# Performance work log

Measured on AMD Instinct MI355X. Metric: run time of the kernel, lower is better.

Reference implementation:

```python
import jax, jax.numpy as jnp
import numpy as np

SEQ = 4096
EMB = 2048
DQ = 2048
DV = 2048

def setup_inputs() -> dict:
    key = jax.random.key(0)
    k1, k2, k3, k4 = jax.random.split(key, 4)
    scale = 1.0 / np.sqrt(EMB)
    return {
        "embedding_word": jax.random.normal(k1, (SEQ, EMB), dtype=jnp.float32),
        "w_q": jax.random.normal(k2, (DQ, EMB), dtype=jnp.float32) * scale,
        "w_k": jax.random.normal(k3, (DQ, EMB), dtype=jnp.float32) * scale,
        "w_v": jax.random.normal(k4, (DV, EMB), dtype=jnp.float32) * scale,
    }

def reference(embedding_word, w_q, w_k, w_v):
    # nn.Linear: y = x @ W.T (bias=False)
    q = embedding_word @ w_q.T            # [S, d_q]
    k = embedding_word @ w_k.T            # [S, d_q]
    v = embedding_word @ w_v.T            # [S, d_v]
    scores = q @ k.T                      # [S, S]
    S = scores.shape[0]
    causal = jnp.tril(jnp.ones((S, S), dtype=bool))  # True = keep
    masked = jnp.where(causal, scores, -jnp.inf)
    weights = jax.nn.softmax(masked / jnp.sqrt(jnp.float32(DQ)), axis=-1)
    return weights @ v                    # [S, d_v]
```

## Files before the change

### kernel.cpp

```cpp
#include <hip/hip_runtime.h>


using u16 = unsigned short;
typedef __bf16 bf16x8 __attribute__((ext_vector_type(8)));
typedef float  f32x4  __attribute__((ext_vector_type(4)));
typedef u16    u16x8  __attribute__((ext_vector_type(8)));

__device__ __forceinline__ u16 f2b(float f) {
  union { float f; unsigned u; } x; x.f = f;
  unsigned r = x.u + 0x7fffu + ((x.u >> 16) & 1u);
  return (u16)(r >> 16);
}
__device__ __forceinline__ float b2f(u16 h) {
  union { unsigned u; float f; } x; x.u = ((unsigned)h) << 16;
  return x.f;
}

#define GLL16(src, dst)                                                        \
  __builtin_amdgcn_global_load_lds(                                            \
      (const __attribute__((address_space(1))) void*)(src),                    \
      (__attribute__((address_space(3))) void*)(dst), 16, 0, 0)

#define MFMA_BF16(a, b, c) __builtin_amdgcn_mfma_f32_16x16x32_bf16(a, b, c, 0, 0, 0)

__global__ __launch_bounds__(256)
void cast_all(const float* __restrict__ x, const float* __restrict__ wq,
              const float* __restrict__ wk, const float* __restrict__ wv,
              u16* __restrict__ dst) {
  const int b = blockIdx.x;
  const float* src;
  size_t off;
  if (b < 4096)      { src = x;  off = (size_t)b * 2048; }
  else if (b < 6144) { src = wq; off = (size_t)(b - 4096) * 2048; }
  else if (b < 8192) { src = wk; off = (size_t)(b - 6144) * 2048; }
  else               { src = wv; off = (size_t)(b - 8192) * 2048; }
  const size_t e = off + (size_t)threadIdx.x * 8;
  float4 a = *(const float4*)(src + e);
  float4 c = *(const float4*)(src + e + 4);
  u16x8 o;
  o[0] = f2b(a.x); o[1] = f2b(a.y); o[2] = f2b(a.z); o[3] = f2b(a.w);
  o[4] = f2b(c.x); o[5] = f2b(c.y); o[6] = f2b(c.z); o[7] = f2b(c.w);
  *(u16x8*)(dst + (size_t)b * 2048 + (size_t)threadIdx.x * 8) = o;
}

__global__ __launch_bounds__(512)
void gemm_qk256(const u16* __restrict__ A, const u16* __restrict__ W,
                u16* __restrict__ Qo, u16* __restrict__ Ko) {
  extern __shared__ char lds[];
  constexpr int NT = 32;
  const int bn = blockIdx.x, bm = blockIdx.y;
  const int tid = threadIdx.x;
  const int w = tid >> 6, lane = tid & 63;
  const int wr = w >> 2, wc = w & 3;
  const int l15 = lane & 15, l4 = lane >> 4;
  const int rs = lane >> 3;
  const int csw = ((lane & 7) ^ rs) << 3;
  const int m0 = bm * 256, n0 = bn * 256;

  const u16* gA = A + (size_t)(m0 + w * 8 + rs) * 2048 + csw;
  const u16* gB = W + (size_t)(n0 + w * 8 + rs) * 2048 + csw;
  char* lw = lds + w * 1024;
  const u16* sm = (const u16*)lds;

  auto stA = [&](int p, int u, int tt) {
    GLL16(gA + (size_t)(u * 64) * 2048 + tt * 64, lw + p * 65536 + u * 8192);
  };
  auto stB = [&](int p, int u, int tt) {
    GLL16(gB + (size_t)(u * 64) * 2048 + tt * 64,
          lw + p * 65536 + 32768 + u * 8192);
  };
  const int swz = (l15 & 7) << 3;
  auto rdA = [&](int p, int m, int kk) -> bf16x8 {
    int u = wr * 2 + (m >> 2);
    int r64 = (m & 3) * 16 + l15;
    int e = p * 32768 + u * 4096 + ((r64 * 64 + kk * 32 + l4 * 8) ^ swz);
    return *(const bf16x8*)&sm[e];
  };
  auto rdB = [&](int p, int n, int kk) -> bf16x8 {
    int e = p * 32768 + 16384 + wc * 4096 +
            (((n * 16 + l15) * 64 + kk * 32 + l4 * 8) ^ swz);
    return *(const bf16x8*)&sm[e];
  };

  f32x4 acc[8][4] = {};
  bf16x8 a0[4][2], a1[4][2], b0[2][2], b1[2][2];

  stA(0,0,0); stA(0,1,0); stA(0,2,0); stA(0,3,0);
  stB(0,0,0); stB(0,1,0); stB(0,2,0); stB(0,3,0);
  stA(1,0,1); stA(1,1,1); stA(1,2,1); stA(1,3,1);
  stB(1,0,1); stB(1,1,1); stB(1,2,1); stB(1,3,1);
  asm volatile("s_waitcnt vmcnt(8)" ::: "memory");
  __builtin_amdgcn_sched_barrier(0);
  __builtin_amdgcn_s_barrier();
#pragma unroll
  for (int m = 0; m < 4; ++m) { a0[m][0] = rdA(0,m,0); a0[m][1] = rdA(0,m,1); }
#pragma unroll
  for (int n = 0; n < 2; ++n) { b0[n][0] = rdB(0,n,0); b0[n][1] = rdB(0,n,1); }

  for (int t = 0; t < NT; ++t) {
    const int p = t & 1;
    const bool pre = (t + 2 < NT);
    b1[0][0] = rdB(p,2,0); b1[0][1] = rdB(p,2,1);
    b1[1][0] = rdB(p,3,0); b1[1][1] = rdB(p,3,1);
    a1[0][0] = rdA(p,4,0); a1[0][1] = rdA(p,4,1);
    asm volatile("s_waitcnt lgkmcnt(6)" ::: "memory");
    __builtin_amdgcn_sched_barrier(0);
    __builtin_amdgcn_s_setprio(1);
#pragma unroll
    for (int m = 0; m < 4; ++m)
#pragma unroll
      for (int n = 0; n < 2; ++n)
#pragma unroll
        for (int kk = 0; kk < 2; ++kk)
          acc[m][n] = MFMA_BF16(a0[m][kk], b0[n][kk], acc[m][n]);
    __builtin_amdgcn_s_setprio(0);
    __builtin_amdgcn_s_barrier();
    if (pre) { stA(p, 0, t + 2); stA(p, 2, t + 2); }
    a1[1][0] = rdA(p,5,0); a1[1][1] = rdA(p,5,1);
    a1[2][0] = rdA(p,6,0); a1[2][1] = rdA(p,6,1);
    a1[3][0] = rdA(p,7,0); a1[3][1] = rdA(p,7,1);
    asm volatile("s_waitcnt lgkmcnt(6)" ::: "memory");
    __builtin_amdgcn_sched_barrier(0);
    __builtin_amdgcn_s_setprio(1);
#pragma unroll
    for (int m = 0; m < 4; ++m)
#pragma unroll
      for (int n = 0; n < 2; ++n)
#pragma unroll
        for (int kk = 0; kk < 2; ++kk)
          acc[m][n + 2] = MFMA_BF16(a0[m][kk], b1[n][kk], acc[m][n + 2]);
    __builtin_amdgcn_s_setprio(0);
    __builtin_amdgcn_s_barrier();
    if (pre) { stB(p, 0, t + 2); stB(p, 1, t + 2); stB(p, 2, t + 2); stB(p, 3, t + 2); }
    asm volatile("s_waitcnt lgkmcnt(0)" ::: "memory");
    __builtin_amdgcn_sched_barrier(0);
    __builtin_amdgcn_s_setprio(1);
#pragma unroll
    for (int m = 0; m < 4; ++m)
#pragma unroll
      for (int n = 0; n < 2; ++n)
#pragma unroll
        for (int kk = 0; kk < 2; ++kk)
          acc[m + 4][n] = MFMA_BF16(a1[m][kk], b0[n][kk], acc[m + 4][n]);
    __builtin_amdgcn_s_setprio(0);
    __builtin_amdgcn_s_barrier();
    if (pre) { stA(p, 1, t + 2); stA(p, 3, t + 2); }
    __builtin_amdgcn_s_setprio(1);
#pragma unroll
    for (int m = 0; m < 4; ++m)
#pragma unroll
      for (int n = 0; n < 2; ++n)
#pragma unroll
        for (int kk = 0; kk < 2; ++kk)
          acc[m + 4][n + 2] = MFMA_BF16(a1[m][kk], b1[n][kk], acc[m + 4][n + 2]);
    __builtin_amdgcn_s_setprio(0);
    if (pre)             { asm volatile("s_waitcnt vmcnt(8)" ::: "memory"); }
    else if (t + 1 < NT) { asm volatile("s_waitcnt vmcnt(0)" ::: "memory"); }
    __builtin_amdgcn_sched_barrier(0);
    __builtin_amdgcn_s_barrier();
    if (t + 1 < NT) {
      const int pn = p ^ 1;
#pragma unroll
      for (int m = 0; m < 4; ++m) { a0[m][0] = rdA(pn,m,0); a0[m][1] = rdA(pn,m,1); }
#pragma unroll
      for (int n = 0; n < 2; ++n) { b0[n][0] = rdB(pn,n,0); b0[n][1] = rdB(pn,n,1); }
    }
  }

  const int row0 = m0 + wr * 128 + l4 * 4;
  if (bn < 8) {
    const int cg0 = bn * 256 + wc * 64 + l15;
#pragma unroll
    for (int m = 0; m < 8; ++m)
#pragma unroll
      for (int n = 0; n < 4; ++n)
#pragma unroll
        for (int j = 0; j < 4; ++j)
          Qo[(size_t)(row0 + m * 16 + j) * 2048 + cg0 + n * 16] = f2b(acc[m][n][j]);
  } else {
    const int cg0 = bn * 256 - 2048 + wc * 64 + l15;
#pragma unroll
    for (int m = 0; m < 8; ++m)
#pragma unroll
      for (int n = 0; n < 4; ++n)
#pragma unroll
        for (int j = 0; j < 4; ++j)
          Ko[(size_t)(row0 + m * 16 + j) * 2048 + cg0 + n * 16] = f2b(acc[m][n][j]);
  }
}

__global__ __launch_bounds__(512)
void gemm_qkv(const u16* __restrict__ A, const u16* __restrict__ W,
              u16* __restrict__ Qo, u16* __restrict__ Ko,
              u16* __restrict__ VTo, int bn_base) {
  extern __shared__ char lds[];
  constexpr int NT = 32;
  const int bn = blockIdx.x + bn_base, bm = blockIdx.y;
  const int tid = threadIdx.x;
  const int w = tid >> 6, lane = tid & 63;
  const int wr = w >> 1, wc = w & 1;
  const int l15 = lane & 15, l4 = lane >> 4;
  const int rs = lane >> 3;
  const int csw = ((lane & 7) ^ rs) << 3;
  const int m0 = bm * 256, n0 = bn * 128;

  const u16* gA = A + (size_t)(m0 + w * 8 + rs) * 2048 + csw;
  const u16* gB = W + (size_t)(n0 + w * 8 + rs) * 2048 + csw;
  char* lw = lds + w * 1024;
  const u16* sm = (const u16*)lds;

  auto stA = [&](int p, int u, int tt) {
    GLL16(gA + (size_t)u * 64 * 2048 + tt * 64, lw + p * 49152 + u * 8192);
  };
  auto stB = [&](int p, int u, int tt) {
    GLL16(gB + (size_t)u * 64 * 2048 + tt * 64, lw + p * 49152 + 32768 + u * 8192);
  };
  const int swz = (l15 & 7) << 3;
  auto rdA = [&](int p, int m, int kk) -> bf16x8 {
    int e = p * 24576 + wr * 4096 + (((m * 16 + l15) * 64 + kk * 32 + l4 * 8) ^ swz);
    return *(const bf16x8*)&sm[e];
  };
  auto rdB = [&](int p, int n, int kk) -> bf16x8 {
    int e = p * 24576 + 16384 + wc * 4096 +
            (((n * 16 + l15) * 64 + kk * 32 + l4 * 8) ^ swz);
    return *(const bf16x8*)&sm[e];
  };

  f32x4 acc[4][4] = {};
  bf16x8 aE[4][2], aO[4][2], b01E[2][2], b01O[2][2], b23E[2][2], b23O[2][2];

  stA(0,0,0); stA(0,1,0); stA(0,2,0); stA(0,3,0); stB(0,0,0); stB(0,1,0);
  stA(1,0,1); stA(1,1,1); stA(1,2,1); stA(1,3,1); stB(1,0,1); stB(1,1,1);
  asm volatile("s_waitcnt vmcnt(6)" ::: "memory");
  __builtin_amdgcn_sched_barrier(0);
  __builtin_amdgcn_s_barrier();
#pragma unroll
  for (int m = 0; m < 4; ++m) { aE[m][0] = rdA(0,m,0); aE[m][1] = rdA(0,m,1); }
#pragma unroll
  for (int n = 0; n < 2; ++n) { b01E[n][0] = rdB(0,n,0); b01E[n][1] = rdB(0,n,1); }
  asm volatile("s_waitcnt lgkmcnt(0)" ::: "memory");
  __builtin_amdgcn_sched_barrier(0);
  __builtin_amdgcn_s_barrier();

  for (int i = 0; i < NT / 2; ++i) {
    const int te = 2 * i, to = 2 * i + 1;
    if (te + 2 < NT) { stA(0,0,te+2); stA(0,1,te+2); stA(0,2,te+2); }
#pragma unroll
    for (int n = 0; n < 2; ++n) { b23E[n][0] = rdB(0,n+2,0); b23E[n][1] = rdB(0,n+2,1); }
    __builtin_amdgcn_s_barrier();
    __builtin_amdgcn_s_setprio(1);
#pragma unroll
    for (int m = 0; m < 4; ++m)
#pragma unroll
      for (int n = 0; n < 2; ++n)
#pragma unroll
        for (int kk = 0; kk < 2; ++kk)
          acc[m][n] = MFMA_BF16(aE[m][kk], b01E[n][kk], acc[m][n]);
    __builtin_amdgcn_s_setprio(0);
    asm volatile("s_waitcnt lgkmcnt(0)" ::: "memory");
    __builtin_amdgcn_sched_barrier(0);
    __builtin_amdgcn_s_barrier();
    if (te + 2 < NT) {
      stA(0,3,te+2); stB(0,0,te+2); stB(0,1,te+2);
      asm volatile("s_waitcnt vmcnt(6)" ::: "memory");
    } else {
      asm volatile("s_waitcnt vmcnt(0)" ::: "memory");
    }
    __builtin_amdgcn_sched_barrier(0);
    __builtin_amdgcn_s_barrier();
#pragma unroll
    for (int m = 0; m < 4; ++m) { aO[m][0] = rdA(1,m,0); aO[m][1] = rdA(1,m,1); }
#pragma unroll
    for (int n = 0; n < 2; ++n) { b01O[n][0] = rdB(1,n,0); b01O[n][1] = rdB(1,n,1); }
    __builtin_amdgcn_s_setprio(1);
#pragma unroll
    for (int m = 0; m < 4; ++m)
#pragma unroll
      for (int n = 0; n < 2; ++n)
#pragma unroll
        for (int kk = 0; kk < 2; ++kk)
          acc[m][n+2] = MFMA_BF16(aE[m][kk], b23E[n][kk], acc[m][n+2]);
    __builtin_amdgcn_s_setprio(0);
    asm volatile("s_waitcnt lgkmcnt(0)" ::: "memory");
    __builtin_amdgcn_sched_barrier(0);
    __builtin_amdgcn_s_barrier();
    if (to + 2 < NT) { stA(1,0,to+2); stA(1,1,to+2); stA(1,2,to+2); }
#pragma unroll
    for (int n = 0; n < 2; ++n) { b23O[n][0] = rdB(1,n+2,0); b23O[n][1] = rdB(1,n+2,1); }
    __builtin_amdgcn_s_barrier();
    __builtin_amdgcn_s_setprio(1);
#pragma unroll
    for (int m = 0; m < 4; ++m)
#pragma unroll
      for (int n = 0; n < 2; ++n)
#pragma unroll
        for (int kk = 0; kk < 2; ++kk)
          acc[m][n] = MFMA_BF16(aO[m][kk], b01O[n][kk], acc[m][n]);
    __builtin_amdgcn_s_setprio(0);
    asm volatile("s_waitcnt lgkmcnt(0)" ::: "memory");
    __builtin_amdgcn_sched_barrier(0);
    __builtin_amdgcn_s_barrier();
    if (to + 2 < NT) {
      stA(1,3,to+2); stB(1,0,to+2); stB(1,1,to+2);
      asm volatile("s_waitcnt vmcnt(6)" ::: "memory");
    } else if (to + 1 < NT) {
      asm volatile("s_waitcnt vmcnt(0)" ::: "memory");
    }
    __builtin_amdgcn_sched_barrier(0);
    __builtin_amdgcn_s_barrier();
    if (to + 1 < NT) {
#pragma unroll
      for (int m = 0; m < 4; ++m) { aE[m][0] = rdA(0,m,0); aE[m][1] = rdA(0,m,1); }
#pragma unroll
      for (int n = 0; n < 2; ++n) { b01E[n][0] = rdB(0,n,0); b01E[n][1] = rdB(0,n,1); }
    }
    __builtin_amdgcn_s_setprio(1);
#pragma unroll
    for (int m = 0; m < 4; ++m)
#pragma unroll
      for (int n = 0; n < 2; ++n)
#pragma unroll
        for (int kk = 0; kk < 2; ++kk)
          acc[m][n+2] = MFMA_BF16(aO[m][kk], b23O[n][kk], acc[m][n+2]);
    __builtin_amdgcn_s_setprio(0);
    asm volatile("s_waitcnt lgkmcnt(0)" ::: "memory");
    __builtin_amdgcn_sched_barrier(0);
    __builtin_amdgcn_s_barrier();
  }

  const int row0 = m0 + wr * 64 + l4 * 4;
  const int cg0 = n0 + wc * 64 + l15;
  if (bn < 16) {
#pragma unroll
    for (int m = 0; m < 4; ++m)
#pragma unroll
      for (int n = 0; n < 4; ++n)
#pragma unroll
        for (int j = 0; j < 4; ++j)
          Qo[(size_t)(row0 + m * 16 + j) * 2048 + cg0 + n * 16] = f2b(acc[m][n][j]);
  } else if (bn < 32) {
#pragma unroll
    for (int m = 0; m < 4; ++m)
#pragma unroll
      for (int n = 0; n < 4; ++n)
#pragma unroll
        for (int j = 0; j < 4; ++j)
          Ko[(size_t)(row0 + m * 16 + j) * 2048 + (cg0 + n * 16 - 2048)] = f2b(acc[m][n][j]);
  } else {
#pragma unroll
    for (int m = 0; m < 4; ++m)
#pragma unroll
      for (int n = 0; n < 4; ++n)
#pragma unroll
        for (int j = 0; j < 4; ++j)
          VTo[(size_t)(cg0 + n * 16 - 4096) * 4096 + row0 + m * 16 + j] = f2b(acc[m][n][j]);
  }
}

template<int MODE>
__global__ __launch_bounds__(256)
void pipe128(const u16* __restrict__ A, const u16* __restrict__ B,
             void* __restrict__ C, float alpha) {
  extern __shared__ char lds[];
  constexpr int LDA = (MODE == 0) ? 2048 : 4096;
  constexpr int LDB = (MODE == 0) ? 2048 : 4096;

  int bm, bn, kt0 = 0;
  bool accum = false;
  if (MODE == 0) {
    const int b = blockIdx.x;
    int r = (int)((sqrtf(8.f * (float)b + 1.f) - 1.f) * 0.5f);
    while ((r + 1) * (r + 2) / 2 <= b) ++r;
    while (r * (r + 1) / 2 > b) --r;
    bm = r; bn = b - r * (r + 1) / 2;
  } else if (MODE == 1) {
    bm = 16 + (blockIdx.x >> 4); bn = blockIdx.x & 15;
  } else {
    const int g = blockIdx.x >> 4;
    bn = blockIdx.x & 15;
    if ((g & 1) == 0) { bm = 31 - (g >> 1); kt0 = 32; accum = true; }
    else              { bm = 15 - (g >> 1); }
  }
  const int NT = (MODE == 0 || MODE == 1) ? 32 : (2 * (bm + 1) - kt0);

  const int tid = threadIdx.x;
  const int w = tid >> 6, lane = tid & 63;
  const int wr = w >> 1, wc = w & 1;
  const int l15 = lane & 15, l4 = lane >> 4;
  const int rs = lane >> 3;
  const int csw = ((lane & 7) ^ rs) << 3;
  const int m0 = bm * 128, n0 = bn * 128;

  const u16* gA = A + (size_t)(m0 + w * 8 + rs) * LDA + csw + (size_t)kt0 * 64;
  const u16* gB = B + (size_t)(n0 + w * 8 + rs) * LDB + csw + (size_t)kt0 * 64;
  const u16* gA0 = gA;
  const u16* gA1 = gA + (size_t)32 * LDA;
  const u16* gA2 = gA + (size_t)64 * LDA;
  const u16* gA3 = gA + (size_t)96 * LDA;
  const u16* gB0 = gB;
  const u16* gB1 = gB + (size_t)32 * LDB;
  const u16* gB2 = gB + (size_t)64 * LDB;
  const u16* gB3 = gB + (size_t)96 * LDB;
  char* lw = lds + w * 1024;
  const u16* sm = (const u16*)lds;
#define PDSTA(P, U) (lw + (P) * 32768 + (U) * 4096)
#define PDSTB(P, U) (lw + (P) * 32768 + 16384 + (U) * 4096)

  const int swz = (l15 & 7) << 3;
  auto rdA = [&](int p, int m, int kk) -> bf16x8 {
    int e = p * 16384 + wr * 4096 + (((m * 16 + l15) * 64 + kk * 32 + l4 * 8) ^ swz);
    return *(const bf16x8*)&sm[e];
  };
  auto rdB = [&](int p, int n, int kk) -> bf16x8 {
    int e = p * 16384 + 8192 + wc * 4096 +
            (((n * 16 + l15) * 64 + kk * 32 + l4 * 8) ^ swz);
    return *(const bf16x8*)&sm[e];
  };

  f32x4 acc[4][4] = {};
  bf16x8 aE[4][2], aO[4][2], b01E[2][2], b01O[2][2], b23E[2][2], b23O[2][2];

  GLL16(gA0, PDSTA(0,0)); GLL16(gA1, PDSTA(0,1));
  GLL16(gA2, PDSTA(0,2)); GLL16(gA3, PDSTA(0,3));
  GLL16(gB0, PDSTB(0,0)); GLL16(gB1, PDSTB(0,1));
  GLL16(gB2, PDSTB(0,2)); GLL16(gB3, PDSTB(0,3));
  GLL16(gA0 + 64, PDSTA(1,0)); GLL16(gA1 + 64, PDSTA(1,1));
  GLL16(gA2 + 64, PDSTA(1,2)); GLL16(gA3 + 64, PDSTA(1,3));
  GLL16(gB0 + 64, PDSTB(1,0)); GLL16(gB1 + 64, PDSTB(1,1));
  GLL16(gB2 + 64, PDSTB(1,2)); GLL16(gB3 + 64, PDSTB(1,3));
  gA0 += 128; gA1 += 128; gA2 += 128; gA3 += 128;
  gB0 += 128; gB1 += 128; gB2 += 128; gB3 += 128;
  asm volatile("s_waitcnt vmcnt(8)" ::: "memory");
  __builtin_amdgcn_sched_barrier(0);
  __builtin_amdgcn_s_barrier();
#pragma unroll
  for (int m = 0; m < 4; ++m) { aE[m][0] = rdA(0,m,0); aE[m][1] = rdA(0,m,1); }
#pragma unroll
  for (int n = 0; n < 2; ++n) { b01E[n][0] = rdB(0,n,0); b01E[n][1] = rdB(0,n,1); }
  asm volatile("s_waitcnt lgkmcnt(0)" ::: "memory");
  __builtin_amdgcn_sched_barrier(0);
  __builtin_amdgcn_s_barrier();

  for (int i = 0; i < (NT >> 1); ++i) {
    const int te = 2 * i, to = 2 * i + 1;
    if (te + 2 < NT) { GLL16(gA0, PDSTA(0,0)); GLL16(gA1, PDSTA(0,1));
                       GLL16(gA2, PDSTA(0,2)); GLL16(gA3, PDSTA(0,3)); }
#pragma unroll
    for (int n = 0; n < 2; ++n) { b23E[n][0] = rdB(0,n+2,0); b23E[n][1] = rdB(0,n+2,1); }
    __builtin_amdgcn_s_barrier();
    __builtin_amdgcn_s_setprio(1);
#pragma unroll
    for (int m = 0; m < 4; ++m)
#pragma unroll
      for (int n = 0; n < 2; ++n)
#pragma unroll
        for (int kk = 0; kk < 2; ++kk)
          acc[m][n] = MFMA_BF16(aE[m][kk], b01E[n][kk], acc[m][n]);
    __builtin_amdgcn_s_setprio(0);
    asm volatile("s_waitcnt lgkmcnt(0)" ::: "memory");
    __builtin_amdgcn_sched_barrier(0);
    __builtin_amdgcn_s_barrier();
    if (te + 2 < NT) {
      GLL16(gB0, PDSTB(0,0)); GLL16(gB1, PDSTB(0,1));
      GLL16(gB2, PDSTB(0,2)); GLL16(gB3, PDSTB(0,3));
      asm volatile("s_waitcnt vmcnt(8)" ::: "memory");
    } else {
      asm volatile("s_waitcnt vmcnt(0)" ::: "memory");
    }
    __builtin_amdgcn_sched_barrier(0);
    __builtin_amdgcn_s_barrier();
#pragma unroll
    for (int m = 0; m < 4; ++m) { aO[m][0] = rdA(1,m,0); aO[m][1] = rdA(1,m,1); }
#pragma unroll
    for (int n = 0; n < 2; ++n) { b01O[n][0] = rdB(1,n,0); b01O[n][1] = rdB(1,n,1); }
    __builtin_amdgcn_s_setprio(1);
#pragma unroll
    for (int m = 0; m < 4; ++m)
#pragma unroll
      for (int n = 0; n < 2; ++n)
#pragma unroll
        for (int kk = 0; kk < 2; ++kk)
          acc[m][n+2] = MFMA_BF16(aE[m][kk], b23E[n][kk], acc[m][n+2]);
    __builtin_amdgcn_s_setprio(0);
    asm volatile("s_waitcnt lgkmcnt(0)" ::: "memory");
    __builtin_amdgcn_sched_barrier(0);
    __builtin_amdgcn_s_barrier();
    if (to + 2 < NT) { GLL16(gA0 + 64, PDSTA(1,0)); GLL16(gA1 + 64, PDSTA(1,1));
                       GLL16(gA2 + 64, PDSTA(1,2)); GLL16(gA3 + 64, PDSTA(1,3)); }
#pragma unroll
    for (int n = 0; n < 2; ++n) { b23O[n][0] = rdB(1,n+2,0); b23O[n][1] = rdB(1,n+2,1); }
    __builtin_amdgcn_s_barrier();
    __builtin_amdgcn_s_setprio(1);
#pragma unroll
    for (int m = 0; m < 4; ++m)
#pragma unroll
      for (int n = 0; n < 2; ++n)
#pragma unroll
        for (int kk = 0; kk < 2; ++kk)
          acc[m][n] = MFMA_BF16(aO[m][kk], b01O[n][kk], acc[m][n]);
    __builtin_amdgcn_s_setprio(0);
    asm volatile("s_waitcnt lgkmcnt(0)" ::: "memory");
    __builtin_amdgcn_sched_barrier(0);
    __builtin_amdgcn_s_barrier();
    if (to + 2 < NT) {
      GLL16(gB0 + 64, PDSTB(1,0)); GLL16(gB1 + 64, PDSTB(1,1));
      GLL16(gB2 + 64, PDSTB(1,2)); GLL16(gB3 + 64, PDSTB(1,3));
      asm volatile("s_waitcnt vmcnt(8)" ::: "memory");
    } else if (to + 1 < NT) {
      asm volatile("s_waitcnt vmcnt(0)" ::: "memory");
    }
    __builtin_amdgcn_sched_barrier(0);
    __builtin_amdgcn_s_barrier();
    if (to + 1 < NT) {
#pragma unroll
      for (int m = 0; m < 4; ++m) { aE[m][0] = rdA(0,m,0); aE[m][1] = rdA(0,m,1); }
#pragma unroll
      for (int n = 0; n < 2; ++n) { b01E[n][0] = rdB(0,n,0); b01E[n][1] = rdB(0,n,1); }
    }
    __builtin_amdgcn_s_setprio(1);
#pragma unroll
    for (int m = 0; m < 4; ++m)
#pragma unroll
      for (int n = 0; n < 2; ++n)
#pragma unroll
        for (int kk = 0; kk < 2; ++kk)
          acc[m][n+2] = MFMA_BF16(aO[m][kk], b23O[n][kk], acc[m][n+2]);
    __builtin_amdgcn_s_setprio(0);
    asm volatile("s_waitcnt lgkmcnt(0)" ::: "memory");
    __builtin_amdgcn_sched_barrier(0);
    __builtin_amdgcn_s_barrier();
    gA0 += 128; gA1 += 128; gA2 += 128; gA3 += 128;
    gB0 += 128; gB1 += 128; gB2 += 128; gB3 += 128;
  }
#undef PDSTA
#undef PDSTB

  const int row0 = m0 + wr * 64 + l4 * 4;
  const int col0 = n0 + wc * 64 + l15;
  if (MODE == 0) {
    u16* Co = (u16*)C;
#pragma unroll
    for (int m = 0; m < 4; ++m)
#pragma unroll
      for (int n = 0; n < 4; ++n)
#pragma unroll
        for (int j = 0; j < 4; ++j)
          Co[(size_t)(row0 + m * 16 + j) * 4096 + col0 + n * 16] =
              f2b(acc[m][n][j] * alpha);
  } else {
    float* Co = (float*)C;
    if (MODE == 2 && accum) {
#pragma unroll
      for (int m = 0; m < 4; ++m)
#pragma unroll
        for (int n = 0; n < 4; ++n)
#pragma unroll
          for (int j = 0; j < 4; ++j)
            Co[(size_t)(row0 + m * 16 + j) * 2048 + col0 + n * 16] += acc[m][n][j];
    } else {
#pragma unroll
      for (int m = 0; m < 4; ++m)
#pragma unroll
        for (int n = 0; n < 4; ++n)
#pragma unroll
          for (int j = 0; j < 4; ++j)
            Co[(size_t)(row0 + m * 16 + j) * 2048 + col0 + n * 16] = acc[m][n][j];
    }
  }
}

__global__ __launch_bounds__(256)
void softmax_causal(u16* __restrict__ S) {
  const int i = blockIdx.x;
  const int t = threadIdx.x;
  u16* row = S + (size_t)i * 4096;
  const int L = ((i >> 7) + 1) << 7;
  const bool act = (t * 16) < L;

  u16x8 r0 = {}, r1 = {};
  if (act) {
    r0 = *(const u16x8*)(row + t * 16);
    r1 = *(const u16x8*)(row + t * 16 + 8);
  }

  float v[16];
  float mx = -__builtin_inff();
#pragma unroll
  for (int c = 0; c < 16; ++c) {
    int j = t * 16 + c;
    float x = b2f(c < 8 ? r0[c] : r1[c - 8]);
    v[c] = (j <= i) ? x : -__builtin_inff();
    mx = fmaxf(mx, v[c]);
  }
#pragma unroll
  for (int off = 32; off >= 1; off >>= 1) mx = fmaxf(mx, __shfl_xor(mx, off));
  __shared__ float red[8];
  if ((t & 63) == 0) red[t >> 6] = mx;
  __syncthreads();
  mx = fmaxf(fmaxf(red[0], red[1]), fmaxf(red[2], red[3]));

  float s = 0.f;
#pragma unroll
  for (int c = 0; c < 16; ++c) {
    float e = exp2f((v[c] - mx) * 1.4426950408889634f);
    v[c] = e;
    s += e;
  }
#pragma unroll
  for (int off = 32; off >= 1; off >>= 1) s += __shfl_xor(s, off);
  if ((t & 63) == 0) red[4 + (t >> 6)] = s;
  __syncthreads();
  s = red[4] + red[5] + red[6] + red[7];
  float inv = 1.0f / s;

  if (act) {
    u16x8 o0, o1;
#pragma unroll
    for (int c = 0; c < 8; ++c) {
      o0[c] = f2b(v[c] * inv);
      o1[c] = f2b(v[c + 8] * inv);
    }
    *(u16x8*)(row + t * 16) = o0;
    *(u16x8*)(row + t * 16 + 8) = o1;
  }
}

extern "C" void kernel_launch(void* const* d_in, const int* in_sizes, int n_in,
                              void* d_out, int out_size, void* d_ws, size_t ws_size,
                              hipStream_t stream) {
  const float* x  = (const float*)d_in[0];
  const float* wq = (const float*)d_in[1];
  const float* wk = (const float*)d_in[2];
  const float* wv = (const float*)d_in[3];

  u16* x_bf  = (u16*)d_ws;
  u16* wq_bf = x_bf  + (size_t)4096 * 2048;
  u16* K_bf  = wq_bf + (size_t)3 * 2048 * 2048;
  u16* VT_bf = K_bf  + (size_t)4096 * 2048;
  u16* S_bf  = VT_bf + (size_t)2048 * 4096;
  u16* Q_bf  = (u16*)d_out;

  const float alpha = 0.022097086912079612f;

  cast_all<<<dim3(10240), 256, 0, stream>>>(x, wq, wk, wv, x_bf);

  gemm_qk256<<<dim3(16, 16), 512, 131072, stream>>>(x_bf, wq_bf, Q_bf, K_bf);
  pipe128<0><<<dim3(528), 256, 65536, stream>>>(Q_bf, K_bf, S_bf, alpha);
  gemm_qkv<<<dim3(16, 16), 512, 98304, stream>>>(x_bf, wq_bf, Q_bf, K_bf, VT_bf, 32);
  softmax_causal<<<dim3(4096), 256, 0, stream>>>(S_bf);
  pipe128<1><<<dim3(256), 256, 65536, stream>>>(S_bf, VT_bf, d_out, 1.0f);
  pipe128<2><<<dim3(512), 256, 65536, stream>>>(S_bf, VT_bf, d_out, 1.0f);
}
```

Measured before the change: 237.2 us.

## Merge V^T projection into the QK^T score launch as extra blocks

Removes the separate gemm_qkv launch that produced V^T and instead appends 512 extra blocks to the pipe128<0> QK^T launch. Those blocks compute V^T = Wv · x^T with the 128x128 tile kernel, writing bf16 with a scale of 1. This lets the V projection fill the GPU alongside the causal score tiles instead of running as its own serialized kernel. The trade-off is that V now uses the smaller-tile 256-thread kernel instead of the 256x128 512-thread one, which may lower its per-block efficiency.

```diff
diff --git a/kernel.cpp b/kernel.cpp
--- a/kernel.cpp
+++ b/kernel.cpp
@@ -189,190 +189,34 @@
   }
 }
 
-__global__ __launch_bounds__(512)
-void gemm_qkv(const u16* __restrict__ A, const u16* __restrict__ W,
-              u16* __restrict__ Qo, u16* __restrict__ Ko,
-              u16* __restrict__ VTo, int bn_base) {
-  extern __shared__ char lds[];
-  constexpr int NT = 32;
-  const int bn = blockIdx.x + bn_base, bm = blockIdx.y;
-  const int tid = threadIdx.x;
-  const int w = tid >> 6, lane = tid & 63;
-  const int wr = w >> 1, wc = w & 1;
-  const int l15 = lane & 15, l4 = lane >> 4;
-  const int rs = lane >> 3;
-  const int csw = ((lane & 7) ^ rs) << 3;
-  const int m0 = bm * 256, n0 = bn * 128;
-
-  const u16* gA = A + (size_t)(m0 + w * 8 + rs) * 2048 + csw;
-  const u16* gB = W + (size_t)(n0 + w * 8 + rs) * 2048 + csw;
-  char* lw = lds + w * 1024;
-  const u16* sm = (const u16*)lds;
-
-  auto stA = [&](int p, int u, int tt) {
-    GLL16(gA + (size_t)u * 64 * 2048 + tt * 64, lw + p * 49152 + u * 8192);
-  };
-  auto stB = [&](int p, int u, int tt) {
-    GLL16(gB + (size_t)u * 64 * 2048 + tt * 64, lw + p * 49152 + 32768 + u * 8192);
-  };
-  const int swz = (l15 & 7) << 3;
-  auto rdA = [&](int p, int m, int kk) -> bf16x8 {
-    int e = p * 24576 + wr * 4096 + (((m * 16 + l15) * 64 + kk * 32 + l4 * 8) ^ swz);
-    return *(const bf16x8*)&sm[e];
-  };
-  auto rdB = [&](int p, int n, int kk) -> bf16x8 {
-    int e = p * 24576 + 16384 + wc * 4096 +
-            (((n * 16 + l15) * 64 + kk * 32 + l4 * 8) ^ swz);
-    return *(const bf16x8*)&sm[e];
-  };
-
-  f32x4 acc[4][4] = {};
-  bf16x8 aE[4][2], aO[4][2], b01E[2][2], b01O[2][2], b23E[2][2], b23O[2][2];
-
-  stA(0,0,0); stA(0,1,0); stA(0,2,0); stA(0,3,0); stB(0,0,0); stB(0,1,0);
-  stA(1,0,1); stA(1,1,1); stA(1,2,1); stA(1,3,1); stB(1,0,1); stB(1,1,1);
-  asm volatile("s_waitcnt vmcnt(6)" ::: "memory");
-  __builtin_amdgcn_sched_barrier(0);
-  __builtin_amdgcn_s_barrier();
-#pragma unroll
-  for (int m = 0; m < 4; ++m) { aE[m][0] = rdA(0,m,0); aE[m][1] = rdA(0,m,1); }
-#pragma unroll
-  for (int n = 0; n < 2; ++n) { b01E[n][0] = rdB(0,n,0); b01E[n][1] = rdB(0,n,1); }
-  asm volatile("s_waitcnt lgkmcnt(0)" ::: "memory");
-  __builtin_amdgcn_sched_barrier(0);
-  __builtin_amdgcn_s_barrier();
-
-  for (int i = 0; i < NT / 2; ++i) {
-    const int te = 2 * i, to = 2 * i + 1;
-    if (te + 2 < NT) { stA(0,0,te+2); stA(0,1,te+2); stA(0,2,te+2); }
-#pragma unroll
-    for (int n = 0; n < 2; ++n) { b23E[n][0] = rdB(0,n+2,0); b23E[n][1] = rdB(0,n+2,1); }
-    __builtin_amdgcn_s_barrier();
-    __builtin_amdgcn_s_setprio(1);
-#pragma unroll
-    for (int m = 0; m < 4; ++m)
-#pragma unroll
-      for (int n = 0; n < 2; ++n)
-#pragma unroll
-        for (int kk = 0; kk < 2; ++kk)
-          acc[m][n] = MFMA_BF16(aE[m][kk], b01E[n][kk], acc[m][n]);
-    __builtin_amdgcn_s_setprio(0);
-    asm volatile("s_waitcnt lgkmcnt(0)" ::: "memory");
-    __builtin_amdgcn_sched_barrier(0);
-    __builtin_amdgcn_s_barrier();
-    if (te + 2 < NT) {
-      stA(0,3,te+2); stB(0,0,te+2); stB(0,1,te+2);
-      asm volatile("s_waitcnt vmcnt(6)" ::: "memory");
-    } else {
-      asm volatile("s_waitcnt vmcnt(0)" ::: "memory");
-    }
-    __builtin_amdgcn_sched_barrier(0);
-    __builtin_amdgcn_s_barrier();
-#pragma unroll
-    for (int m = 0; m < 4; ++m) { aO[m][0] = rdA(1,m,0); aO[m][1] = rdA(1,m,1); }
-#pragma unroll
-    for (int n = 0; n < 2; ++n) { b01O[n][0] = rdB(1,n,0); b01O[n][1] = rdB(1,n,1); }
-    __builtin_amdgcn_s_setprio(1);
-#pragma unroll
-    for (int m = 0; m < 4; ++m)
-#pragma unroll
-      for (int n = 0; n < 2; ++n)
-#pragma unroll
-        for (int kk = 0; kk < 2; ++kk)
-          acc[m][n+2] = MFMA_BF16(aE[m][kk], b23E[n][kk], acc[m][n+2]);
-    __builtin_amdgcn_s_setprio(0);
-    asm volatile("s_waitcnt lgkmcnt(0)" ::: "memory");
-    __builtin_amdgcn_sched_barrier(0);
-    __builtin_amdgcn_s_barrier();
-    if (to + 2 < NT) { stA(1,0,to+2); stA(1,1,to+2); stA(1,2,to+2); }
-#pragma unroll
-    for (int n = 0; n < 2; ++n) { b23O[n][0] = rdB(1,n+2,0); b23O[n][1] = rdB(1,n+2,1); }
-    __builtin_amdgcn_s_barrier();
-    __builtin_amdgcn_s_setprio(1);
-#pragma unroll
-    for (int m = 0; m < 4; ++m)
-#pragma unroll
-      for (int n = 0; n < 2; ++n)
-#pragma unroll
-        for (int kk = 0; kk < 2; ++kk)
-          acc[m][n] = MFMA_BF16(aO[m][kk], b01O[n][kk], acc[m][n]);
-    __builtin_amdgcn_s_setprio(0);
-    asm volatile("s_waitcnt lgkmcnt(0)" ::: "memory");
-    __builtin_amdgcn_sched_barrier(0);
-    __builtin_amdgcn_s_barrier();
-    if (to + 2 < NT) {
-      stA(1,3,to+2); stB(1,0,to+2); stB(1,1,to+2);
-      asm volatile("s_waitcnt vmcnt(6)" ::: "memory");
-    } else if (to + 1 < NT) {
-      asm volatile("s_waitcnt vmcnt(0)" ::: "memory");
-    }
-    __builtin_amdgcn_sched_barrier(0);
-    __builtin_amdgcn_s_barrier();
-    if (to + 1 < NT) {
-#pragma unroll
-      for (int m = 0; m < 4; ++m) { aE[m][0] = rdA(0,m,0); aE[m][1] = rdA(0,m,1); }
-#pragma unroll
-      for (int n = 0; n < 2; ++n) { b01E[n][0] = rdB(0,n,0); b01E[n][1] = rdB(0,n,1); }
-    }
-    __builtin_amdgcn_s_setprio(1);
-#pragma unroll
-    for (int m = 0; m < 4; ++m)
-#pragma unroll
-      for (int n = 0; n < 2; ++n)
-#pragma unroll
-        for (int kk = 0; kk < 2; ++kk)
-          acc[m][n+2] = MFMA_BF16(aO[m][kk], b23O[n][kk], acc[m][n+2]);
-    __builtin_amdgcn_s_setprio(0);
-    asm volatile("s_waitcnt lgkmcnt(0)" ::: "memory");
-    __builtin_amdgcn_sched_barrier(0);
-    __builtin_amdgcn_s_barrier();
-  }
-
-  const int row0 = m0 + wr * 64 + l4 * 4;
-  const int cg0 = n0 + wc * 64 + l15;
-  if (bn < 16) {
-#pragma unroll
-    for (int m = 0; m < 4; ++m)
-#pragma unroll
-      for (int n = 0; n < 4; ++n)
-#pragma unroll
-        for (int j = 0; j < 4; ++j)
-          Qo[(size_t)(row0 + m * 16 + j) * 2048 + cg0 + n * 16] = f2b(acc[m][n][j]);
-  } else if (bn < 32) {
-#pragma unroll
-    for (int m = 0; m < 4; ++m)
-#pragma unroll
-      for (int n = 0; n < 4; ++n)
-#pragma unroll
-        for (int j = 0; j < 4; ++j)
-          Ko[(size_t)(row0 + m * 16 + j) * 2048 + (cg0 + n * 16 - 2048)] = f2b(acc[m][n][j]);
-  } else {
-#pragma unroll
-    for (int m = 0; m < 4; ++m)
-#pragma unroll
-      for (int n = 0; n < 4; ++n)
-#pragma unroll
-        for (int j = 0; j < 4; ++j)
-          VTo[(size_t)(cg0 + n * 16 - 4096) * 4096 + row0 + m * 16 + j] = f2b(acc[m][n][j]);
-  }
-}
-
 template<int MODE>
 __global__ __launch_bounds__(256)
 void pipe128(const u16* __restrict__ A, const u16* __restrict__ B,
-             void* __restrict__ C, float alpha) {
+             void* __restrict__ C, float alpha,
+             const u16* __restrict__ A2, const u16* __restrict__ B2,
+             u16* __restrict__ C2) {
   extern __shared__ char lds[];
   constexpr int LDA = (MODE == 0) ? 2048 : 4096;
   constexpr int LDB = (MODE == 0) ? 2048 : 4096;
 
   int bm, bn, kt0 = 0;
   bool accum = false;
+  const u16* Ap = A;
+  const u16* Bp = B;
+  u16* Cbf = (u16*)C;
+  float scale = alpha;
   if (MODE == 0) {
-    const int b = blockIdx.x;
-    int r = (int)((sqrtf(8.f * (float)b + 1.f) - 1.f) * 0.5f);
-    while ((r + 1) * (r + 2) / 2 <= b) ++r;
-    while (r * (r + 1) / 2 > b) --r;
-    bm = r; bn = b - r * (r + 1) / 2;
+    int b = blockIdx.x;
+    if (b < 528) {
+      int r = (int)((sqrtf(8.f * (float)b + 1.f) - 1.f) * 0.5f);
+      while ((r + 1) * (r + 2) / 2 <= b) ++r;
+      while (r * (r + 1) / 2 > b) --r;
+      bm = r; bn = b - r * (r + 1) / 2;
+    } else {
+      b -= 528;
+      bm = b >> 5; bn = b & 31;
+      Ap = A2; Bp = B2; Cbf = C2; scale = 1.0f;
+    }
   } else if (MODE == 1) {
     bm = 16 + (blockIdx.x >> 4); bn = blockIdx.x & 15;
   } else {
@@ -391,8 +235,8 @@
   const int csw = ((lane & 7) ^ rs) << 3;
   const int m0 = bm * 128, n0 = bn * 128;
 
-  const u16* gA = A + (size_t)(m0 + w * 8 + rs) * LDA + csw + (size_t)kt0 * 64;
-  const u16* gB = B + (size_t)(n0 + w * 8 + rs) * LDB + csw + (size_t)kt0 * 64;
+  const u16* gA = Ap + (size_t)(m0 + w * 8 + rs) * LDA + csw + (size_t)kt0 * 64;
+  const u16* gB = Bp + (size_t)(n0 + w * 8 + rs) * LDB + csw + (size_t)kt0 * 64;
   const u16* gA0 = gA;
   const u16* gA1 = gA + (size_t)32 * LDA;
   const u16* gA2 = gA + (size_t)64 * LDA;
@@ -538,15 +382,14 @@
   const int row0 = m0 + wr * 64 + l4 * 4;
   const int col0 = n0 + wc * 64 + l15;
   if (MODE == 0) {
-    u16* Co = (u16*)C;
 #pragma unroll
     for (int m = 0; m < 4; ++m)
 #pragma unroll
       for (int n = 0; n < 4; ++n)
 #pragma unroll
         for (int j = 0; j < 4; ++j)
-          Co[(size_t)(row0 + m * 16 + j) * 4096 + col0 + n * 16] =
-              f2b(acc[m][n][j] * alpha);
+          Cbf[(size_t)(row0 + m * 16 + j) * 4096 + col0 + n * 16] =
+              f2b(acc[m][n][j] * scale);
   } else {
     float* Co = (float*)C;
     if (MODE == 2 && accum) {
@@ -635,6 +478,7 @@
 
   u16* x_bf  = (u16*)d_ws;
   u16* wq_bf = x_bf  + (size_t)4096 * 2048;
+  u16* wv_bf = wq_bf + (size_t)2 * 2048 * 2048;
   u16* K_bf  = wq_bf + (size_t)3 * 2048 * 2048;
   u16* VT_bf = K_bf  + (size_t)4096 * 2048;
   u16* S_bf  = VT_bf + (size_t)2048 * 4096;
@@ -645,9 +489,11 @@
   cast_all<<<dim3(10240), 256, 0, stream>>>(x, wq, wk, wv, x_bf);
 
   gemm_qk256<<<dim3(16, 16), 512, 131072, stream>>>(x_bf, wq_bf, Q_bf, K_bf);
-  pipe128<0><<<dim3(528), 256, 65536, stream>>>(Q_bf, K_bf, S_bf, alpha);
-  gemm_qkv<<<dim3(16, 16), 512, 98304, stream>>>(x_bf, wq_bf, Q_bf, K_bf, VT_bf, 32);
+  pipe128<0><<<dim3(1040), 256, 65536, stream>>>(
+      Q_bf, K_bf, S_bf, alpha, wv_bf, x_bf, VT_bf);
   softmax_causal<<<dim3(4096), 256, 0, stream>>>(S_bf);
-  pipe128<1><<<dim3(256), 256, 65536, stream>>>(S_bf, VT_bf, d_out, 1.0f);
-  pipe128<2><<<dim3(512), 256, 65536, stream>>>(S_bf, VT_bf, d_out, 1.0f);
-}
+  pipe128<1><<<dim3(256), 256, 65536, stream>>>(
+      S_bf, VT_bf, d_out, 1.0f, nullptr, nullptr, nullptr);
+  pipe128<2><<<dim3(512), 256, 65536, stream>>>(
+      S_bf, VT_bf, d_out, 1.0f, nullptr, nullptr, nullptr);
+}
```

Result: faster. 229.5 us (median of 2 runs) (-3.2%).
